# Kernel tuning notes

Measured on AMD Instinct MI355X. Metric: run time of the kernel, lower is better.

The kernel has to match this reference:

```python
import jax, jax.numpy as jnp
import numpy as np

KS = 3           # kernel size (conv1, conv2, deform conv)
PAD = 1          # k//2 padding for the dense convs and deform zero-padding
DIM = 256
B, H, W = 4, 64, 64
N = KS * KS      # number of sampling points per output pixel


def conv2d(x, w, b=None, pad=PAD, stride=1):
    out = jax.lax.conv_general_dilated(
        x, w, (stride, stride), [(pad, pad), (pad, pad)],
        dimension_numbers=('NCHW', 'OIHW', 'NCHW'))
    if b is not None:
        out = out + b[None, :, None, None]
    return out


def deform_conv(x, p_w, p_b, dw):
    # DeformConv2d (deform-conv-v2 style, modulation=False)
    b, c, h, w = x.shape
    offset = conv2d(x, p_w, p_b, pad=1)                     # (b, 2N, h, w)
    xp = jnp.pad(x, ((0, 0), (0, 0), (PAD, PAD), (PAD, PAD)))
    Hp, Wp = h + 2 * PAD, w + 2 * PAD

    # kernel-relative offsets p_n: rows first, then cols (row-major flatten)
    r = jnp.arange(-(KS - 1) // 2, (KS - 1) // 2 + 1, dtype=x.dtype)
    pnx, pny = jnp.meshgrid(r, r, indexing='ij')
    p_n = jnp.concatenate([pnx.ravel(), pny.ravel()])       # (2N,)

    # base grid p_0 starts at 1 (consistent with zero padding of 1)
    gy, gx = jnp.meshgrid(jnp.arange(1, h + 1, dtype=x.dtype),
                          jnp.arange(1, w + 1, dtype=x.dtype), indexing='ij')
    p0 = jnp.concatenate([jnp.tile(gy[..., None], (1, 1, N)),
                          jnp.tile(gx[..., None], (1, 1, N))], axis=-1)  # (h,w,2N)

    p = jnp.transpose(offset, (0, 2, 3, 1)) + p_n + p0      # (b,h,w,2N)
    px, py = p[..., :N], p[..., N:]
    fx, fy = jnp.floor(px), jnp.floor(py)
    qlx = jnp.clip(fx, 0, Hp - 1)
    qly = jnp.clip(fy, 0, Wp - 1)
    qrx = jnp.clip(fx + 1, 0, Hp - 1)
    qry = jnp.clip(fy + 1, 0, Wp - 1)
    px = jnp.clip(px, 0, Hp - 1)
    py = jnp.clip(py, 0, Wp - 1)

    # bilinear weights
    g_lt = (1 + qlx - px) * (1 + qly - py)
    g_rb = (1 - qrx + px) * (1 - qry + py)
    g_lb = (1 + qlx - px) * (1 - qry + py)
    g_rt = (1 - qrx + px) * (1 + qly - py)

    xf = xp.reshape(b, c, Hp * Wp)

    def gather(qx, qy):
        idx = (qx.astype(jnp.int32) * Wp + qy.astype(jnp.int32)).reshape(b, -1)
        return jax.vmap(lambda xb, ib: xb[:, ib])(xf, idx).reshape(b, c, h, w, N)

    x_off = (g_lt[:, None] * gather(qlx, qly) + g_rb[:, None] * gather(qrx, qry)
           + g_lb[:, None] * gather(qlx, qry) + g_rt[:, None] * gather(qrx, qly))

    # (b,c,h,w,N) -> (b,c,h*ks,w*ks): kernel row expands h, kernel col expands w
    x_off = x_off.reshape(b, c, h, w, KS, KS).transpose(0, 1, 2, 4, 3, 5)
    x_off = x_off.reshape(b, c, h * KS, w * KS)
    return conv2d(x_off, dw, None, pad=0, stride=KS)       # (b, c, h, w)


def setup_inputs() -> dict:
    key = jax.random.key(0)
    ks = jax.random.split(key, 8)
    s = 1.0 / np.sqrt(DIM * KS * KS)
    return {
        'x':   jax.random.normal(ks[0], (B, DIM, H, W), jnp.float32),
        'w1':  jax.random.normal(ks[1], (DIM, DIM, KS, KS), jnp.float32) * s,
        'b1':  jax.random.normal(ks[2], (DIM,), jnp.float32) * 0.01,
        'w2':  jax.random.normal(ks[3], (DIM, DIM, KS, KS), jnp.float32) * s,
        'b2':  jax.random.normal(ks[4], (DIM,), jnp.float32) * 0.01,
        'p_w': jax.random.normal(ks[5], (2 * N, DIM, 3, 3), jnp.float32) * (0.05 * s),
        'p_b': jnp.zeros((2 * N,), jnp.float32),
        'dw':  jax.random.normal(ks[6], (DIM, DIM, KS, KS), jnp.float32) * s,
    }


def reference(x, w1, b1, w2, b2, p_w, p_b, dw):
    res = jax.nn.relu(conv2d(x, w1, b1, pad=PAD))   # conv1 + ReLU
    res = res + x                                   # residual 1
    res = conv2d(res, w2, b2, pad=PAD)              # conv2
    res = deform_conv(res, p_w, p_b, dw)            # deformable conv
    return res + x                                  # residual 2
```

## Files before the change

### kernel.cpp

```cpp
#include <hip/hip_runtime.h>

#define HW 64
#define NB 4
#define CH 256

typedef __attribute__((address_space(1))) const void* gptr_t;
typedef __attribute__((address_space(3))) void* lptr_t;
typedef __attribute__((ext_vector_type(8))) short bf8v;
typedef __attribute__((ext_vector_type(4))) float f32x4;

__device__ __forceinline__ void gll16(const void* g, void* l) {
  __builtin_amdgcn_global_load_lds((gptr_t)g, (lptr_t)l, 16, 0, 0);
}
__device__ __forceinline__ ushort f2b(float f) {
  union { float f; uint u; } v; v.f = f;
  uint r = v.u + 0x7FFF + ((v.u >> 16) & 1);
  return (ushort)(r >> 16);
}
__device__ __forceinline__ uint cvt_pk_bf16(float lo, float hi) {
  uint r;
  asm("v_cvt_pk_bf16_f32 %0, %1, %2" : "=v"(r) : "v"(lo), "v"(hi));
  return r;
}
__device__ __forceinline__ float asf(uint u) {
  union { uint u; float f; } v; v.u = u; return v.f;
}

__device__ __forceinline__ void combine_store(
    const uint4& c0, const uint4& c1, const uint4& c2, const uint4& c3,
    const float4& gw, ushort* dst)
{
  uint o[4];
  const uint* p0 = (const uint*)&c0; const uint* p1 = (const uint*)&c1;
  const uint* p2 = (const uint*)&c2; const uint* p3 = (const uint*)&c3;
  #pragma unroll
  for (int w = 0; w < 4; ++w) {
    const float lo = gw.x * asf(p0[w] << 16) + gw.y * asf(p1[w] << 16)
                   + gw.z * asf(p2[w] << 16) + gw.w * asf(p3[w] << 16);
    const float hi = gw.x * asf(p0[w] & 0xffff0000u) + gw.y * asf(p1[w] & 0xffff0000u)
                   + gw.z * asf(p2[w] & 0xffff0000u) + gw.w * asf(p3[w] & 0xffff0000u);
    o[w] = cvt_pk_bf16(lo, hi);
  }
  uint4 r; r.x = o[0]; r.y = o[1]; r.z = o[2]; r.w = o[3];
  *(uint4*)dst = r;
}

__global__ __launch_bounds__(256) void prep_k(
    const float* __restrict__ x,
    const float* __restrict__ w1, const float* __restrict__ w2,
    const float* __restrict__ dw, const float* __restrict__ pw,
    const float* __restrict__ pb,
    ushort* __restrict__ xpad, ushort* __restrict__ res1, ushort* __restrict__ res2,
    ushort* __restrict__ wpk1, ushort* __restrict__ wpk2,
    ushort* __restrict__ dwpk, ushort* __restrict__ wpkO, float* __restrict__ pbias)
{
  __shared__ float tile[64][261];
  const int bid = blockIdx.x, t = threadIdx.x;

  if (bid < 256) {
    const int b = bid >> 6, i = bid & 63;
    const int wave = t >> 6, l = t & 63;
    const float* src = x + (size_t)b * CH * 4096 + (size_t)i * 64;
    for (int cc = 0; cc < 64; ++cc) {
      const int c = cc * 4 + wave;
      tile[l][c] = src[(size_t)c * 4096 + l];
    }
    __syncthreads();
    const int c0 = (t & 31) * 8;
    #pragma unroll
    for (int jj = 0; jj < 8; ++jj) {
      const int j = (t >> 5) + jj * 8;
      const float4 v0 = *(const float4*)&tile[j][c0];
      const float4 v1 = *(const float4*)&tile[j][c0 + 4];
      uint4 o;
      o.x = cvt_pk_bf16(v0.x, v0.y);
      o.y = cvt_pk_bf16(v0.z, v0.w);
      o.z = cvt_pk_bf16(v1.x, v1.y);
      o.w = cvt_pk_bf16(v1.z, v1.w);
      *(uint4*)&xpad[((size_t)b * 4356 + (i + 1) * 66 + (j + 1)) * 256 + c0] = o;
    }
  } else if (bid < 1156) {
    const int id = (bid - 256) * 256 + t;
    if (id < 3 * 73728) {
      const int tsel = id / 73728, r = id % 73728;
      const int kc = r & 3, o = (r >> 2) & 255, ct = r >> 10;
      const int cb = ct / 9, tap = ct % 9;
      const float* w = (tsel == 0) ? w1 : (tsel == 1) ? w2 : dw;
      const float* s = w + ((size_t)o * CH + cb * 32 + kc * 8) * 9 + tap;
      ushort* d = ((tsel == 0) ? wpk1 : (tsel == 1) ? wpk2 : dwpk) + (size_t)r * 8;
      #pragma unroll
      for (int j = 0; j < 8; ++j) d[j] = f2b(s[j * 9]);
    } else if (id < 3 * 73728 + 9216) {
      const int r = id - 3 * 73728;
      const int kc = r & 3, o = (r >> 2) & 31, ct = r >> 7;
      const int cb = ct / 9, tap = ct % 9;
      ushort* d = wpkO + (size_t)r * 8;
      if (o < 18) {
        const float* s = pw + ((size_t)o * CH + cb * 32 + kc * 8) * 9 + tap;
        #pragma unroll
        for (int j = 0; j < 8; ++j) d[j] = f2b(s[j * 9]);
      } else {
        #pragma unroll
        for (int j = 0; j < 8; ++j) d[j] = 0;
      }
    }
    if (id < 32) pbias[id] = (id < 18) ? pb[id] : 0.f;
  } else {
    const int v = bid - 1156;
    const int buf = v >> 2, b = v & 3;
    ushort* base = (buf == 0 ? xpad : buf == 1 ? res1 : res2) + (size_t)b * 4356 * 256;
    uint4 z; z.x = 0; z.y = 0; z.z = 0; z.w = 0;
    for (int u = t; u < 260 * 32; u += 256) {
      const int p = u >> 5, k = u & 31;
      int r, cc;
      if (p < 66)       { r = 0;       cc = p; }
      else if (p < 132) { r = 65;      cc = p - 66; }
      else if (p < 196) { r = p - 131; cc = 0; }
      else              { r = p - 195; cc = 65; }
      *(uint4*)&base[((size_t)r * 66 + cc) * 256 + k * 8] = z;
    }
  }
}

template<int OTOT, int OUTMODE>
__global__ __launch_bounds__(256, 2) void conv_mfma(
    const ushort* __restrict__ apad, const ushort* __restrict__ wpk,
    const float* __restrict__ bias, const float* __restrict__ xres,
    void* __restrict__ outp)
{
  __shared__ __align__(16) ushort patch[2][6336];
  const int t = threadIdx.x, wave = t >> 6, l = t & 63;
  const int ot  = (OTOT == 256) ? (blockIdx.x >> 8) : 0;
  const int rem = blockIdx.x & 255;
  const int b = rem >> 6, i = rem & 63;
  const int ln = l & 15, kc8 = (l >> 4) * 8;

  constexpr int FO = 2;
  constexpr int FP = (OTOT == 256) ? 4 : 1;
  const int oS  = (OTOT == 256) ? (ot * 128 + wave * 32) : 0;
  const int pxB = (OTOT == 256) ? 0 : (wave * 16);

  const ushort* rowbase = apad + ((size_t)(b * 66 + i) * 66) * 256;

  f32x4 acc[FO][FP];
  #pragma unroll
  for (int a = 0; a < FO; ++a)
    #pragma unroll
    for (int d = 0; d < FP; ++d) acc[a][d] = (f32x4){0.f, 0.f, 0.f, 0.f};

  #define STAGE(buf, cb)                                                        \
    _Pragma("unroll")                                                           \
    for (int it = 0; it < 4; ++it) {                                            \
      const int e = t + it * 256;                                               \
      if (it < 3 || t < 24) {                                                   \
        const int r = e / 264, u = e - r * 264;                                 \
        const int p = r * 66 + (u >> 2);                                        \
        const int sl = (u & 3) ^ ((p >> 1) & 3);                                \
        const ushort* s = rowbase + (size_t)p * 256 + (cb) * 32 + sl * 8;       \
        gll16(s, (ushort*)&patch[buf][0] + (size_t)e * 8);                      \
      }                                                                         \
    }

  STAGE(0, 0)
  for (int cb = 0; cb < 8; ++cb) {
    __syncthreads();
    const ushort* pbuf = &patch[cb & 1][0];
    #pragma unroll
    for (int ch = 0; ch < 3; ++ch) {
      bf8v wfr[3][FO];
      #pragma unroll
      for (int q = 0; q < 3; ++q) {
        const int tap = ch * 3 + q;
        #pragma unroll
        for (int fo = 0; fo < FO; ++fo)
          wfr[q][fo] = *(const bf8v*)&wpk[((size_t)((cb * 9 + tap) * OTOT) + oS + fo * 16 + ln) * 32 + kc8];
      }
      if (ch == 2 && cb < 7) { STAGE((cb + 1) & 1, cb + 1) }
      __builtin_amdgcn_s_setprio(1);
      #pragma unroll
      for (int q = 0; q < 3; ++q) {
        const int tap = ch * 3 + q;
        const int ky = tap / 3, kx = tap % 3;
        #pragma unroll
        for (int fp = 0; fp < FP; ++fp) {
          const int px = pxB + fp * 16 + ln;
          const int pix = ky * 66 + px + kx;
          const int sl = (l >> 4) ^ ((pix >> 1) & 3);
          const bf8v pf = *(const bf8v*)&pbuf[pix * 32 + sl * 8];
          #pragma unroll
          for (int fo = 0; fo < FO; ++fo)
            acc[fo][fp] = __builtin_amdgcn_mfma_f32_16x16x32_bf16(wfr[q][fo], pf, acc[fo][fp], 0, 0, 0);
        }
      }
      __builtin_amdgcn_s_setprio(0);
    }
  }
  #undef STAGE

  #pragma unroll
  for (int fo = 0; fo < FO; ++fo) {
    #pragma unroll
    for (int fp = 0; fp < FP; ++fp) {
      const f32x4 a = acc[fo][fp];
      const int o = oS + fo * 16 + (l >> 4) * 4;
      const int j = pxB + fp * 16 + ln;
      const float4 bv = *(const float4*)&bias[o];
      float v0 = a[0] + bv.x, v1 = a[1] + bv.y, v2 = a[2] + bv.z, v3 = a[3] + bv.w;
      if (OUTMODE == 0) {
        const size_t xb = (((size_t)b * CH + o) * HW + i) * HW + j;
        v0 = fmaxf(v0, 0.f) + xres[xb];
        v1 = fmaxf(v1, 0.f) + xres[xb + 4096];
        v2 = fmaxf(v2, 0.f) + xres[xb + 8192];
        v3 = fmaxf(v3, 0.f) + xres[xb + 12288];
      }
      if (OUTMODE == 2) {
        float* op = (float*)outp + ((size_t)b * 4096 + i * 64 + j) * 32 + o;
        float4 r; r.x = v0; r.y = v1; r.z = v2; r.w = v3;
        *(float4*)op = r;
      } else {
        ushort* op = (ushort*)outp + ((size_t)b * 4356 + (i + 1) * 66 + (j + 1)) * 256 + o;
        ushort4 s; s.x = f2b(v0); s.y = f2b(v1); s.z = f2b(v2); s.w = f2b(v3);
        *(ushort4*)op = s;
      }
    }
  }
}

__global__ __launch_bounds__(512, 2) void deform_mfma(
    const ushort* __restrict__ res2pad, const float* __restrict__ offs,
    const ushort* __restrict__ dwpk, const float* __restrict__ x,
    float* __restrict__ out)
{
  __shared__ __align__(16) ushort samp[2][18432];
  __shared__ __align__(16) int    tblI[576 * 4];
  __shared__ __align__(16) float  tblW[576 * 4];

  const int t = threadIdx.x, wave = t >> 6, l = t & 63;
  const int blk = (blockIdx.x & 7) * 32 + (blockIdx.x >> 3);
  const int b = blk >> 6, i = blk & 63;
  const int ln = l & 15, kc8 = (l >> 4) * 8;
  const int oS = wave * 32;

  #pragma unroll
  for (int k2 = 0; k2 < 2; ++k2) {
    const int e = t + k2 * 512;
    if (e < 576) {
      const int n = e >> 6, j = e & 63;
      const int ki = n / 3, kj = n % 3;
      const float offr = offs[((size_t)(b * 64 + i) * 64 + j) * 32 + n];
      const float offc = offs[((size_t)(b * 64 + i) * 64 + j) * 32 + 9 + n];
      const float prow = offr + (float)(ki - 1) + (float)(i + 1);
      const float pcol = offc + (float)(kj - 1) + (float)(j + 1);
      const float fx = floorf(prow), fy = floorf(pcol);
      const float qlx = fminf(fmaxf(fx, 0.f), 65.f);
      const float qly = fminf(fmaxf(fy, 0.f), 65.f);
      const float qrx = fminf(fmaxf(fx + 1.f, 0.f), 65.f);
      const float qry = fminf(fmaxf(fy + 1.f, 0.f), 65.f);
      const float pr  = fminf(fmaxf(prow, 0.f), 65.f);
      const float pc  = fminf(fmaxf(pcol, 0.f), 65.f);
      tblI[e * 4 + 0] = ((int)qlx * 66 + (int)qly) * 512;
      tblI[e * 4 + 1] = ((int)qrx * 66 + (int)qry) * 512;
      tblI[e * 4 + 2] = ((int)qlx * 66 + (int)qry) * 512;
      tblI[e * 4 + 3] = ((int)qrx * 66 + (int)qly) * 512;
      tblW[e * 4 + 0] = (1.f + qlx - pr) * (1.f + qly - pc);
      tblW[e * 4 + 1] = (1.f - qrx + pr) * (1.f - qry + pc);
      tblW[e * 4 + 2] = (1.f + qlx - pr) * (1.f - qry + pc);
      tblW[e * 4 + 3] = (1.f - qrx + pr) * (1.f + qly - pc);
    }
  }

  f32x4 acc[2][4];
  #pragma unroll
  for (int a = 0; a < 2; ++a)
    #pragma unroll
    for (int d = 0; d < 4; ++d) acc[a][d] = (f32x4){0.f, 0.f, 0.f, 0.f};

  const char* res2b = (const char*)(res2pad + (size_t)b * 4356 * 256);

  #define SAMPLE_CB(cb_, buf_)                                                  \
    _Pragma("unroll")                                                           \
    for (int k = 0; k < 5; ++k) {                                               \
      if (k < 4 || t < 256) {                                                   \
        const int u = t + k * 512;                                              \
        const int e = u >> 2, i16 = u & 3;                                      \
        const int4 iv = *(const int4*)&tblI[e * 4];                             \
        const float4 gw = *(const float4*)&tblW[e * 4];                         \
        const char* gb = res2b + (cb_) * 64 + i16 * 16;                         \
        const uint4 c0 = *(const uint4*)(gb + iv.x);                            \
        const uint4 c1 = *(const uint4*)(gb + iv.y);                            \
        const uint4 c2 = *(const uint4*)(gb + iv.z);                            \
        const uint4 c3 = *(const uint4*)(gb + iv.w);                            \
        const int sl = i16 ^ ((e >> 1) & 3);                                    \
        combine_store(c0, c1, c2, c3, gw, &samp[buf_][(size_t)e * 32 + sl * 8]);\
      }                                                                         \
    }

  __syncthreads();
  SAMPLE_CB(0, 0)
  __syncthreads();

  const int rsl = ((l >> 4) ^ ((ln >> 1) & 3)) * 8;

  for (int cb = 0; cb < 8; ++cb) {
    const ushort* sb = &samp[cb & 1][0];
    const ushort* wbase = dwpk + (size_t)(cb * 9) * 256 * 32;

    #pragma unroll
    for (int ch = 0; ch < 3; ++ch) {
      bf8v bfr[3][2];
      #pragma unroll
      for (int q = 0; q < 3; ++q)
        #pragma unroll
        for (int fo = 0; fo < 2; ++fo)
          bfr[q][fo] = *(const bf8v*)&wbase[((size_t)((ch * 3 + q) * 256) + oS + fo * 16 + ln) * 32 + kc8];
      __builtin_amdgcn_s_setprio(1);
      #pragma unroll
      for (int q = 0; q < 3; ++q) {
        const int tap = ch * 3 + q;
        #pragma unroll
        for (int fp = 0; fp < 4; ++fp) {
          const bf8v af = *(const bf8v*)&sb[(tap * 64 + fp * 16 + ln) * 32 + rsl];
          #pragma unroll
          for (int fo = 0; fo < 2; ++fo)
            acc[fo][fp] = __builtin_amdgcn_mfma_f32_16x16x32_bf16(af, bfr[q][fo], acc[fo][fp], 0, 0, 0);
        }
      }
      __builtin_amdgcn_s_setprio(0);
    }

    if (cb < 7) { SAMPLE_CB(cb + 1, (cb + 1) & 1) }
    __syncthreads();
  }
  #undef SAMPLE_CB

  #pragma unroll
  for (int fo = 0; fo < 2; ++fo) {
    #pragma unroll
    for (int fp = 0; fp < 4; ++fp) {
      const f32x4 a = acc[fo][fp];
      const int o = oS + fo * 16 + ln;
      const int j0 = fp * 16 + (l >> 4) * 4;
      const size_t base = (((size_t)b * CH + o) * HW + i) * HW + j0;
      const float4 xv = *(const float4*)&x[base];
      float4 r; r.x = a[0] + xv.x; r.y = a[1] + xv.y; r.z = a[2] + xv.z; r.w = a[3] + xv.w;
      *(float4*)&out[base] = r;
    }
  }
}

extern "C" void kernel_launch(void* const* d_in, const int* in_sizes, int n_in,
                              void* d_out, int out_size, void* d_ws, size_t ws_size,
                              hipStream_t stream) {
  (void)in_sizes; (void)n_in; (void)out_size; (void)ws_size;
  const float* x  = (const float*)d_in[0];
  const float* w1 = (const float*)d_in[1];
  const float* b1 = (const float*)d_in[2];
  const float* w2 = (const float*)d_in[3];
  const float* b2 = (const float*)d_in[4];
  const float* pw = (const float*)d_in[5];
  const float* pb = (const float*)d_in[6];
  const float* dw = (const float*)d_in[7];
  float* out = (float*)d_out;

  char* w = (char*)d_ws;
  size_t off = 0;
  auto carve = [&](size_t bytes) { char* p = w + off; off += (bytes + 255) & ~(size_t)255; return p; };
  ushort* xpad  = (ushort*)carve(8929280);
  ushort* res1  = (ushort*)carve(8929280);
  ushort* res2  = (ushort*)carve(8929280);
  ushort* wpk1  = (ushort*)carve(1179648);
  ushort* wpk2  = (ushort*)carve(1179648);
  ushort* wpkO  = (ushort*)carve(147456);
  ushort* dwpk  = (ushort*)carve(1179648);
  float*  pbias = (float*) carve(256);
  float*  offs  = (float*) carve(2097152);

  prep_k<<<1168, 256, 0, stream>>>(x, w1, w2, dw, pw, pb,
                                   xpad, res1, res2, wpk1, wpk2, dwpk, wpkO, pbias);
  conv_mfma<256, 0><<<512, 256, 0, stream>>>(xpad, wpk1, b1, x, res1);
  conv_mfma<256, 1><<<512, 256, 0, stream>>>(res1, wpk2, b2, nullptr, res2);
  conv_mfma<32, 2><<<256, 256, 0, stream>>>(res2, wpkO, pbias, nullptr, offs);
  deform_mfma<<<NB * HW, 512, 0, stream>>>(res2, offs, dwpk, x, out);
}
```

Baseline: 122.0 us.

## Merge output-channel halves into one 512-thread block and double-buffer weight fragments

The two dense conv launches now use 256 blocks of 512 threads. Each block covers all 256 output channels for one row, so the input patch is staged once per row instead of twice. Weight fragment loads are software-pipelined across two register sets, so the next chunk's loads overlap the current chunk's MFMAs. The cost is fewer blocks (256 on a large GPU) with possibly lower occupancy and higher register pressure.

After: 124.5 us. +2.1%, slower.

```diff
diff --git a/kernel.cpp b/kernel.cpp
--- a/kernel.cpp
+++ b/kernel.cpp
@@ -123,21 +123,20 @@
 }
 
 template<int OTOT, int OUTMODE>
-__global__ __launch_bounds__(256, 2) void conv_mfma(
+__global__ __launch_bounds__(512, 2) void conv_mfma(
     const ushort* __restrict__ apad, const ushort* __restrict__ wpk,
     const float* __restrict__ bias, const float* __restrict__ xres,
     void* __restrict__ outp)
 {
+  constexpr int NT = (OTOT == 256) ? 512 : 256;
   __shared__ __align__(16) ushort patch[2][6336];
   const int t = threadIdx.x, wave = t >> 6, l = t & 63;
-  const int ot  = (OTOT == 256) ? (blockIdx.x >> 8) : 0;
-  const int rem = blockIdx.x & 255;
-  const int b = rem >> 6, i = rem & 63;
+  const int b = (blockIdx.x & 255) >> 6, i = blockIdx.x & 63;
   const int ln = l & 15, kc8 = (l >> 4) * 8;
 
   constexpr int FO = 2;
   constexpr int FP = (OTOT == 256) ? 4 : 1;
-  const int oS  = (OTOT == 256) ? (ot * 128 + wave * 32) : 0;
+  const int oS  = (OTOT == 256) ? (wave * 32) : 0;
   const int pxB = (OTOT == 256) ? 0 : (wave * 16);
 
   const ushort* rowbase = apad + ((size_t)(b * 66 + i) * 66) * 256;
@@ -150,9 +149,9 @@
 
   #define STAGE(buf, cb)                                                        \
     _Pragma("unroll")                                                           \
-    for (int it = 0; it < 4; ++it) {                                            \
-      const int e = t + it * 256;                                               \
-      if (it < 3 || t < 24) {                                                   \
+    for (int it = 0; it < ((NT == 512) ? 2 : 4); ++it) {                        \
+      const int e = t + it * NT;                                                \
+      if (e < 792) {                                                            \
         const int r = e / 264, u = e - r * 264;                                 \
         const int p = r * 66 + (u >> 2);                                        \
         const int sl = (u & 3) ^ ((p >> 1) & 3);                                \
@@ -161,40 +160,49 @@
       }                                                                         \
     }
 
+  #define LOADW(dst, cb_, ch_)                                                  \
+    _Pragma("unroll")                                                           \
+    for (int q = 0; q < 3; ++q) {                                               \
+      _Pragma("unroll")                                                         \
+      for (int fo = 0; fo < FO; ++fo)                                           \
+        dst[q][fo] = *(const bf8v*)&wpk[((size_t)(((cb_) * 9 + (ch_) * 3 + q) * OTOT) + oS + fo * 16 + ln) * 32 + kc8]; \
+    }
+
+  #define MFMACH(ch_, wset) {                                                   \
+      __builtin_amdgcn_s_setprio(1);                                            \
+      _Pragma("unroll")                                                         \
+      for (int q = 0; q < 3; ++q) {                                             \
+        const int tap = (ch_) * 3 + q;                                          \
+        const int ky = tap / 3, kx = tap % 3;                                   \
+        _Pragma("unroll")                                                       \
+        for (int fp = 0; fp < FP; ++fp) {                                       \
+          const int px = pxB + fp * 16 + ln;                                    \
+          const int pix = ky * 66 + px + kx;                                    \
+          const int sl = (l >> 4) ^ ((pix >> 1) & 3);                           \
+          const bf8v pf = *(const bf8v*)&pbuf[pix * 32 + sl * 8];               \
+          _Pragma("unroll")                                                     \
+          for (int fo = 0; fo < FO; ++fo)                                       \
+            acc[fo][fp] = __builtin_amdgcn_mfma_f32_16x16x32_bf16(wset[q][fo], pf, acc[fo][fp], 0, 0, 0); \
+        }                                                                       \
+      }                                                                         \
+      __builtin_amdgcn_s_setprio(0);                                            \
+    }
+
   STAGE(0, 0)
   for (int cb = 0; cb < 8; ++cb) {
     __syncthreads();
     const ushort* pbuf = &patch[cb & 1][0];
-    #pragma unroll
-    for (int ch = 0; ch < 3; ++ch) {
-      bf8v wfr[3][FO];
-      #pragma unroll
-      for (int q = 0; q < 3; ++q) {
-        const int tap = ch * 3 + q;
-        #pragma unroll
-        for (int fo = 0; fo < FO; ++fo)
-          wfr[q][fo] = *(const bf8v*)&wpk[((size_t)((cb * 9 + tap) * OTOT) + oS + fo * 16 + ln) * 32 + kc8];
-      }
-      if (ch == 2 && cb < 7) { STAGE((cb + 1) & 1, cb + 1) }
-      __builtin_amdgcn_s_setprio(1);
-      #pragma unroll
-      for (int q = 0; q < 3; ++q) {
-        const int tap = ch * 3 + q;
-        const int ky = tap / 3, kx = tap % 3;
-        #pragma unroll
-        for (int fp = 0; fp < FP; ++fp) {
-          const int px = pxB + fp * 16 + ln;
-          const int pix = ky * 66 + px + kx;
-          const int sl = (l >> 4) ^ ((pix >> 1) & 3);
-          const bf8v pf = *(const bf8v*)&pbuf[pix * 32 + sl * 8];
-          #pragma unroll
-          for (int fo = 0; fo < FO; ++fo)
-            acc[fo][fp] = __builtin_amdgcn_mfma_f32_16x16x32_bf16(wfr[q][fo], pf, acc[fo][fp], 0, 0, 0);
-        }
-      }
-      __builtin_amdgcn_s_setprio(0);
-    }
-  }
+    bf8v wA[3][FO], wB[3][FO];
+    LOADW(wA, cb, 0)
+    if (cb < 7) { STAGE((cb + 1) & 1, cb + 1) }
+    LOADW(wB, cb, 1)
+    MFMACH(0, wA)
+    LOADW(wA, cb, 2)
+    MFMACH(1, wB)
+    MFMACH(2, wA)
+  }
+  #undef MFMACH
+  #undef LOADW
   #undef STAGE
 
   #pragma unroll
@@ -377,8 +385,8 @@
 
   prep_k<<<1168, 256, 0, stream>>>(x, w1, w2, dw, pw, pb,
                                    xpad, res1, res2, wpk1, wpk2, dwpk, wpkO, pbias);
-  conv_mfma<256, 0><<<512, 256, 0, stream>>>(xpad, wpk1, b1, x, res1);
-  conv_mfma<256, 1><<<512, 256, 0, stream>>>(res1, wpk2, b2, nullptr, res2);
+  conv_mfma<256, 0><<<256, 512, 0, stream>>>(xpad, wpk1, b1, x, res1);
+  conv_mfma<256, 1><<<256, 512, 0, stream>>>(res1, wpk2, b2, nullptr, res2);
   conv_mfma<32, 2><<<256, 256, 0, stream>>>(res2, wpkO, pbias, nullptr, offs);
   deform_mfma<<<NB * HW, 512, 0, stream>>>(res2, offs, dwpk, x, out);
 }
```
